# Kernel optimization log

Measured on AMD Instinct MI355X. Metric: run time of the kernel, lower is better.

The kernel has to match this reference:

```python
import jax, jax.numpy as jnp
import numpy as np

BS, SEQ, D, H = 2, 2048, 1024, 16
HD = D // H  # head_dim = 64


def setup_inputs() -> dict:
    key = jax.random.key(0)
    kx, kw = jax.random.split(key)
    x = jax.random.normal(kx, (BS, SEQ, D), dtype=jnp.float32)
    # qkv Linear: weight [3D, D] (xavier_normal), bias zeros
    std = float(np.sqrt(2.0 / (D + 3 * D)))
    W_qkv = jax.random.normal(kw, (3 * D, D), dtype=jnp.float32) * std
    b_qkv = jnp.zeros((3 * D,), dtype=jnp.float32)
    return {"x": x, "W_qkv": W_qkv, "b_qkv": b_qkv}


def reference(x, W_qkv, b_qkv):
    bs, seq_len, embed_dim = x.shape
    # fused QKV projection: [bs, seq, 3D]
    qkv = x @ W_qkv.T + b_qkv
    qkv = qkv.reshape(bs, seq_len, 3, H, HD)
    qkv = jnp.transpose(qkv, (2, 0, 3, 1, 4))  # [3, bs, H, seq, HD]
    Q, K, V = qkv[0], qkv[1], qkv[2]
    # past_kv is None -> total_len == seq_len, past_len == 0
    scores = jnp.einsum("bhqd,bhkd->bhqk", Q, K) / jnp.sqrt(jnp.float32(HD))
    # causal mask: True above diagonal -> -inf
    mask = jnp.triu(jnp.ones((seq_len, seq_len), dtype=bool), k=1)
    scores = jnp.where(mask[None, None, :, :], -jnp.inf, scores)
    probs = jax.nn.softmax(scores, axis=-1)
    # attn_dropout = 0.0 (eval) -> identity
    out = jnp.einsum("bhqk,bhkd->bhqd", probs, V)
    out = jnp.transpose(out, (0, 2, 1, 3)).reshape(bs, seq_len, embed_dim)
    return (out, (K, V))
```

## Files before the change

kernel.cpp:

```cpp
#include <hip/hip_runtime.h>

typedef __bf16 bf16_t;
typedef __bf16 bf16x8 __attribute__((ext_vector_type(8)));
typedef float f32x4 __attribute__((ext_vector_type(4)));

__device__ __forceinline__ bf16_t f2bf(float f) {
  unsigned u = __float_as_uint(f);
  u += 0x7fffu + ((u >> 16) & 1u);
  unsigned short s = (unsigned short)(u >> 16);
  union { unsigned short s; bf16_t b; } cv; cv.s = s; return cv.b;
}

__device__ __forceinline__ void gl16(const void* g, void* l) {
  __builtin_amdgcn_global_load_lds(
      (const __attribute__((address_space(1))) void*)g,
      (__attribute__((address_space(3))) void*)l,
      16, 0, 0);
}

__global__ __launch_bounds__(256) void cvt_kernel(const float* __restrict__ src,
                                                  bf16_t* __restrict__ dst, int n8) {
  int i = blockIdx.x * 256 + threadIdx.x;
  if (i >= n8) return;
  const float4* s = (const float4*)src + (size_t)i * 2;
  float4 a = s[0], b = s[1];
  bf16x8 o;
  o[0] = f2bf(a.x); o[1] = f2bf(a.y); o[2] = f2bf(a.z); o[3] = f2bf(a.w);
  o[4] = f2bf(b.x); o[5] = f2bf(b.y); o[6] = f2bf(b.z); o[7] = f2bf(b.w);
  *((bf16x8*)dst + i) = o;
}

#define GEMM_K 1024
__global__ __launch_bounds__(256) void qkv_gemm(
    const bf16_t* __restrict__ A,
    const bf16_t* __restrict__ B,
    const float* __restrict__ bias,
    float* __restrict__ Ko, float* __restrict__ Vo,
    bf16_t* __restrict__ Qb, bf16_t* __restrict__ Kb,
    bf16_t* __restrict__ Vt)
{
  __shared__ bf16_t lsA[128 * 32];
  __shared__ bf16_t lsB[128 * 32];
  const int tid = threadIdx.x;
  const int lane = tid & 63;
  const int ln = lane & 15, qd = lane >> 4;
  const int wid = tid >> 6;
  const int wm = wid & 1, wn = wid >> 1;
  const int bm = blockIdx.x & 31, bn = blockIdx.x >> 5;
  const int m0 = bm * 128, n0 = bn * 128;

  f32x4 acc[4][4] = {};

  const int c0 = tid, c1 = tid + 256;
  const bf16_t* ga0 = A + (size_t)(m0 + (c0 >> 2)) * GEMM_K + (c0 & 3) * 8;
  const bf16_t* ga1 = A + (size_t)(m0 + (c1 >> 2)) * GEMM_K + (c1 & 3) * 8;
  const bf16_t* gb0 = B + (size_t)(n0 + (c0 >> 2)) * GEMM_K + (c0 & 3) * 8;
  const bf16_t* gb1 = B + (size_t)(n0 + (c1 >> 2)) * GEMM_K + (c1 & 3) * 8;
  bf16_t* la0 = &lsA[c0 * 8];
  bf16_t* la1 = &lsA[c1 * 8];
  bf16_t* lb0 = &lsB[c0 * 8];
  bf16_t* lb1 = &lsB[c1 * 8];

  for (int k0 = 0; k0 < GEMM_K; k0 += 32) {
    __syncthreads();
    gl16(ga0 + k0, la0);
    gl16(ga1 + k0, la1);
    gl16(gb0 + k0, lb0);
    gl16(gb1 + k0, lb1);
    __syncthreads();
    bf16x8 af[4], bf[4];
#pragma unroll
    for (int mi = 0; mi < 4; ++mi)
      af[mi] = *(const bf16x8*)&lsA[(wm * 64 + mi * 16 + ln) * 32 + qd * 8];
#pragma unroll
    for (int ni = 0; ni < 4; ++ni)
      bf[ni] = *(const bf16x8*)&lsB[(wn * 64 + ni * 16 + ln) * 32 + qd * 8];
#pragma unroll
    for (int mi = 0; mi < 4; ++mi)
#pragma unroll
      for (int ni = 0; ni < 4; ++ni)
        acc[mi][ni] = __builtin_amdgcn_mfma_f32_16x16x32_bf16(af[mi], bf[ni], acc[mi][ni], 0, 0, 0);
  }

  const int sec = n0 >> 10;
#pragma unroll
  for (int mi = 0; mi < 4; ++mi) {
#pragma unroll
    for (int ni = 0; ni < 4; ++ni) {
      const int colg = n0 + wn * 64 + ni * 16 + ln;
      const float bv = bias[colg];
      const int cc = colg & 1023, h = cc >> 6, hd = cc & 63;
#pragma unroll
      for (int r = 0; r < 4; ++r) {
        const int mg = m0 + wm * 64 + mi * 16 + qd * 4 + r;
        const int b = mg >> 11, s = mg & 2047;
        const float val = acc[mi][ni][r] + bv;
        const size_t idx = ((size_t)((b * 16 + h) * 2048 + s)) * 64 + hd;
        if (sec == 0) {
          Qb[idx] = f2bf(val);
        } else if (sec == 1) {
          Ko[idx] = val;
          Kb[idx] = f2bf(val);
        } else {
          Vo[idx] = val;
          Vt[((size_t)(b * 16 + h) * 64 + hd) * 2048 + s] = f2bf(val);
        }
      }
    }
  }
}

#define LP_STRIDE 72
__global__ __launch_bounds__(256) void attn_kernel(
    const bf16_t* __restrict__ Qb,
    const bf16_t* __restrict__ Kb,
    const bf16_t* __restrict__ Vt,
    float* __restrict__ Oacc,
    float* __restrict__ lacc)
{
  __shared__ bf16_t lq[128 * 64];
  __shared__ bf16_t lk[64 * 64];
  __shared__ bf16_t lv[64 * 64];
  __shared__ bf16_t lp[128 * LP_STRIDE];
  const int tid = threadIdx.x;
  const int lane = tid & 63, ln = lane & 15, qd = lane >> 4;
  const int w = tid >> 6;

  const int bh = blockIdx.x / 40;
  int c = blockIdx.x % 40;
  int it = 0;
#pragma unroll
  for (int t = 0; t < 16; ++t) {
    int nc = (2 * t + 9) >> 3;
    if (c < nc) { it = t; break; }
    c -= nc;
  }
  const int jt0 = c * 8;
  const int jt1 = min(jt0 + 8, 2 * it + 2);
  const int b = bh >> 4, h = bh & 15;

  const bf16_t* qbase = Qb + (size_t)bh * 2048 * 64 + (size_t)it * 128 * 64;
  const bf16_t* kbase = Kb + (size_t)bh * 2048 * 64;
  const bf16_t* vbase = Vt + (size_t)bh * 64 * 2048;

#pragma unroll
  for (int i = 0; i < 4; ++i) {
    int cc = tid + i * 256;
    gl16(qbase + cc * 8, &lq[cc * 8]);
  }
  __syncthreads();
  bf16x8 afq[2][2];
#pragma unroll
  for (int kk = 0; kk < 2; ++kk)
#pragma unroll
    for (int mi = 0; mi < 2; ++mi)
      afq[kk][mi] = *(const bf16x8*)&lq[(w * 32 + mi * 16 + ln) * 64 + kk * 32 + qd * 8];

  f32x4 oc[2][4] = {};
  float lsum[2][4] = {};
  const float C1 = 0.125f * 1.44269504f;

  for (int jt = jt0; jt < jt1; ++jt) {
    __syncthreads();
    {
      const bf16_t* kt = kbase + (size_t)jt * 64 * 64;
      int cc = tid, c2 = tid + 256;
      gl16(kt + cc * 8, &lk[cc * 8]);
      gl16(kt + c2 * 8, &lk[c2 * 8]);
      gl16(vbase + (size_t)(cc >> 3) * 2048 + jt * 64 + (cc & 7) * 8, &lv[cc * 8]);
      gl16(vbase + (size_t)(c2 >> 3) * 2048 + jt * 64 + (c2 & 7) * 8, &lv[c2 * 8]);
    }
    __syncthreads();

    f32x4 sa[2][4] = {};
#pragma unroll
    for (int kk = 0; kk < 2; ++kk) {
      bf16x8 bfk[4];
#pragma unroll
      for (int ni = 0; ni < 4; ++ni)
        bfk[ni] = *(const bf16x8*)&lk[(ni * 16 + ln) * 64 + kk * 32 + qd * 8];
#pragma unroll
      for (int mi = 0; mi < 2; ++mi)
#pragma unroll
        for (int ni = 0; ni < 4; ++ni)
          sa[mi][ni] = __builtin_amdgcn_mfma_f32_16x16x32_bf16(afq[kk][mi], bfk[ni], sa[mi][ni], 0, 0, 0);
    }

    const bool diag = (jt >= 2 * it);
#pragma unroll
    for (int mi = 0; mi < 2; ++mi) {
#pragma unroll
      for (int r = 0; r < 4; ++r) {
        const int rowg = it * 128 + w * 32 + mi * 16 + qd * 4 + r;
#pragma unroll
        for (int ni = 0; ni < 4; ++ni) {
          float sv = sa[mi][ni][r] * C1;
          if (diag) {
            int colg = jt * 64 + ni * 16 + ln;
            if (colg > rowg) sv = -10000.f;
          }
          float p = __builtin_amdgcn_exp2f(sv);
          sa[mi][ni][r] = p;
          lsum[mi][r] += p;
        }
      }
    }

#pragma unroll
    for (int mi = 0; mi < 2; ++mi)
#pragma unroll
      for (int ni = 0; ni < 4; ++ni)
#pragma unroll
        for (int r = 0; r < 4; ++r)
          lp[(w * 32 + mi * 16 + qd * 4 + r) * LP_STRIDE + ni * 16 + ln] = f2bf(sa[mi][ni][r]);

#pragma unroll
    for (int kk = 0; kk < 2; ++kk) {
      bf16x8 afp[2], bfv[4];
#pragma unroll
      for (int mi = 0; mi < 2; ++mi)
        afp[mi] = *(const bf16x8*)&lp[(w * 32 + mi * 16 + ln) * LP_STRIDE + kk * 32 + qd * 8];
#pragma unroll
      for (int ni = 0; ni < 4; ++ni)
        bfv[ni] = *(const bf16x8*)&lv[(ni * 16 + ln) * 64 + kk * 32 + qd * 8];
#pragma unroll
      for (int mi = 0; mi < 2; ++mi)
#pragma unroll
        for (int ni = 0; ni < 4; ++ni)
          oc[mi][ni] = __builtin_amdgcn_mfma_f32_16x16x32_bf16(afp[mi], bfv[ni], oc[mi][ni], 0, 0, 0);
    }
  }

#pragma unroll
  for (int mi = 0; mi < 2; ++mi) {
#pragma unroll
    for (int r = 0; r < 4; ++r) {
      float ls = lsum[mi][r];
      ls += __shfl_xor(ls, 1);
      ls += __shfl_xor(ls, 2);
      ls += __shfl_xor(ls, 4);
      ls += __shfl_xor(ls, 8);
      const int rowg = it * 128 + w * 32 + mi * 16 + qd * 4 + r;
      if (ln == 0) atomicAdd(lacc + bh * 2048 + rowg, ls);
#pragma unroll
      for (int ni = 0; ni < 4; ++ni) {
        const int colh = ni * 16 + ln;
        atomicAdd(Oacc + (size_t)(b * 2048 + rowg) * 1024 + h * 64 + colh, oc[mi][ni][r]);
      }
    }
  }
}

__global__ __launch_bounds__(256) void norm_kernel(float* __restrict__ Oacc,
                                                   const float* __restrict__ lacc) {
  const size_t f = ((size_t)blockIdx.x * 256 + threadIdx.x) * 4;
  const int d = (int)(f & 1023);
  const int s = (int)((f >> 10) & 2047);
  const int b = (int)(f >> 21);
  const int h = d >> 6;
  const float l = lacc[(((size_t)b * 16 + h) << 11) | s];
  const float inv = 1.0f / l;
  float4* p = (float4*)(Oacc + f);
  float4 v = *p;
  v.x *= inv; v.y *= inv; v.z *= inv; v.w *= inv;
  *p = v;
}

extern "C" void kernel_launch(void* const* d_in, const int* in_sizes, int n_in,
                              void* d_out, int out_size, void* d_ws, size_t ws_size,
                              hipStream_t stream) {
  const float* x = (const float*)d_in[0];
  const float* W = (const float*)d_in[1];
  const float* bq = (const float*)d_in[2];
  float* out = (float*)d_out;
  float* Ko = out + 4194304;
  float* Vo = out + 8388608;
  char* ws = (char*)d_ws;
  bf16_t* xb = (bf16_t*)ws;
  bf16_t* wb = (bf16_t*)(ws + 8388608);
  bf16_t* Qb = (bf16_t*)(ws + 14680064);
  bf16_t* Kb = (bf16_t*)(ws + 23068672);
  bf16_t* Vt = (bf16_t*)(ws + 31457280);
  float*  lacc = (float*)(ws + 39845888);

  hipMemsetAsync(out, 0, 4194304 * sizeof(float), stream);
  hipMemsetAsync(lacc, 0, 65536 * sizeof(float), stream);
  hipLaunchKernelGGL(cvt_kernel, dim3(2048), dim3(256), 0, stream, x, xb, 524288);
  hipLaunchKernelGGL(cvt_kernel, dim3(1536), dim3(256), 0, stream, W, wb, 393216);
  hipLaunchKernelGGL(qkv_gemm, dim3(768), dim3(256), 0, stream, xb, wb, bq, Ko, Vo, Qb, Kb, Vt);
  hipLaunchKernelGGL(attn_kernel, dim3(1280), dim3(256), 0, stream, Qb, Kb, Vt, out, lacc);
  hipLaunchKernelGGL(norm_kernel, dim3(4096), dim3(256), 0, stream, out, lacc);
}
```

Baseline: 195.0 us.

## Swizzle LDS layouts, tile K/V contiguously, drop split-K attention atomics and norm pass

Converted inputs and the GEMM's Q/K/V outputs are written in XOR-swizzled, 64-row tiled layouts, so LDS fragment reads avoid bank conflicts and K/V tiles load as contiguous chunks. The attention kernel no longer splits the key range across blocks. Each of the 512 blocks handles one full query tile in longest-first order and writes normalized output directly. This removes the memsets, the atomicAdd reductions and the separate norm kernel. The cost is fewer blocks with unbalanced per-block work, which may lower parallelism on the tail.

```diff
diff --git a/kernel.cpp b/kernel.cpp
--- a/kernel.cpp
+++ b/kernel.cpp
@@ -27,7 +27,10 @@
   bf16x8 o;
   o[0] = f2bf(a.x); o[1] = f2bf(a.y); o[2] = f2bf(a.z); o[3] = f2bf(a.w);
   o[4] = f2bf(b.x); o[5] = f2bf(b.y); o[6] = f2bf(b.z); o[7] = f2bf(b.w);
-  *((bf16x8*)dst + i) = o;
+  const int row = i >> 7, jr = i & 127;
+  const int g = jr >> 2, jj = jr & 3;
+  const int dstc = (row << 7) + (g << 2) + (jj ^ ((row >> 1) & 3));
+  *((bf16x8*)dst + dstc) = o;
 }
 
 #define GEMM_K 1024
@@ -48,6 +51,7 @@
   const int wm = wid & 1, wn = wid >> 1;
   const int bm = blockIdx.x & 31, bn = blockIdx.x >> 5;
   const int m0 = bm * 128, n0 = bn * 128;
+  const int qs = qd ^ ((ln >> 1) & 3);
 
   f32x4 acc[4][4] = {};
 
@@ -71,10 +75,10 @@
     bf16x8 af[4], bf[4];
 #pragma unroll
     for (int mi = 0; mi < 4; ++mi)
-      af[mi] = *(const bf16x8*)&lsA[(wm * 64 + mi * 16 + ln) * 32 + qd * 8];
+      af[mi] = *(const bf16x8*)&lsA[(wm * 64 + mi * 16 + ln) * 32 + qs * 8];
 #pragma unroll
     for (int ni = 0; ni < 4; ++ni)
-      bf[ni] = *(const bf16x8*)&lsB[(wn * 64 + ni * 16 + ln) * 32 + qd * 8];
+      bf[ni] = *(const bf16x8*)&lsB[(wn * 64 + ni * 16 + ln) * 32 + qs * 8];
 #pragma unroll
     for (int mi = 0; mi < 4; ++mi)
 #pragma unroll
@@ -95,15 +99,20 @@
         const int mg = m0 + wm * 64 + mi * 16 + qd * 4 + r;
         const int b = mg >> 11, s = mg & 2047;
         const float val = acc[mi][ni][r] + bv;
-        const size_t idx = ((size_t)((b * 16 + h) * 2048 + s)) * 64 + hd;
+        const int bhi = b * 16 + h;
+        const size_t pidx = ((size_t)(bhi * 2048 + s)) * 64 + hd;
+        const size_t sidx = (size_t)bhi * 131072 + (size_t)(s >> 6) * 4096 +
+                            (size_t)(s & 63) * 64 + (((hd >> 3) ^ (s & 7)) << 3) + (hd & 7);
         if (sec == 0) {
-          Qb[idx] = f2bf(val);
+          Qb[sidx] = f2bf(val);
         } else if (sec == 1) {
-          Ko[idx] = val;
-          Kb[idx] = f2bf(val);
+          Ko[pidx] = val;
+          Kb[sidx] = f2bf(val);
         } else {
-          Vo[idx] = val;
-          Vt[((size_t)(b * 16 + h) * 64 + hd) * 2048 + s] = f2bf(val);
+          Vo[pidx] = val;
+          const size_t vidx = (size_t)bhi * 131072 + (size_t)(s >> 6) * 4096 +
+                              (size_t)hd * 64 + ((((s >> 3) & 7) ^ (hd & 7)) << 3) + (s & 7);
+          Vt[vidx] = f2bf(val);
         }
       }
     }
@@ -115,8 +124,7 @@
     const bf16_t* __restrict__ Qb,
     const bf16_t* __restrict__ Kb,
     const bf16_t* __restrict__ Vt,
-    float* __restrict__ Oacc,
-    float* __restrict__ lacc)
+    float* __restrict__ Out)
 {
   __shared__ bf16_t lq[128 * 64];
   __shared__ bf16_t lk[64 * 64];
@@ -126,22 +134,15 @@
   const int lane = tid & 63, ln = lane & 15, qd = lane >> 4;
   const int w = tid >> 6;
 
-  const int bh = blockIdx.x / 40;
-  int c = blockIdx.x % 40;
-  int it = 0;
-#pragma unroll
-  for (int t = 0; t < 16; ++t) {
-    int nc = (2 * t + 9) >> 3;
-    if (c < nc) { it = t; break; }
-    c -= nc;
-  }
-  const int jt0 = c * 8;
-  const int jt1 = min(jt0 + 8, 2 * it + 2);
+  const int bidx = blockIdx.x;
+  const int bh = bidx & 31;
+  const int x = bidx >> 5;
+  const int it = (bidx < 256) ? (15 - x) : (x - 8);
   const int b = bh >> 4, h = bh & 15;
 
-  const bf16_t* qbase = Qb + (size_t)bh * 2048 * 64 + (size_t)it * 128 * 64;
-  const bf16_t* kbase = Kb + (size_t)bh * 2048 * 64;
-  const bf16_t* vbase = Vt + (size_t)bh * 64 * 2048;
+  const bf16_t* qbase = Qb + (size_t)bh * 131072 + (size_t)it * 8192;
+  const bf16_t* kbase = Kb + (size_t)bh * 131072;
+  const bf16_t* vbase = Vt + (size_t)bh * 131072;
 
 #pragma unroll
   for (int i = 0; i < 4; ++i) {
@@ -153,22 +154,27 @@
 #pragma unroll
   for (int kk = 0; kk < 2; ++kk)
 #pragma unroll
-    for (int mi = 0; mi < 2; ++mi)
-      afq[kk][mi] = *(const bf16x8*)&lq[(w * 32 + mi * 16 + ln) * 64 + kk * 32 + qd * 8];
+    for (int mi = 0; mi < 2; ++mi) {
+      const int row = w * 32 + mi * 16 + ln;
+      afq[kk][mi] = *(const bf16x8*)&lq[(row >> 6) * 4096 + (row & 63) * 64 +
+                                        (((kk * 4 + qd) ^ (ln & 7)) << 3)];
+    }
 
   f32x4 oc[2][4] = {};
   float lsum[2][4] = {};
   const float C1 = 0.125f * 1.44269504f;
 
-  for (int jt = jt0; jt < jt1; ++jt) {
+  const int jt1 = 2 * it + 2;
+  for (int jt = 0; jt < jt1; ++jt) {
     __syncthreads();
     {
-      const bf16_t* kt = kbase + (size_t)jt * 64 * 64;
+      const bf16_t* kt = kbase + (size_t)jt * 4096;
+      const bf16_t* vt = vbase + (size_t)jt * 4096;
       int cc = tid, c2 = tid + 256;
       gl16(kt + cc * 8, &lk[cc * 8]);
       gl16(kt + c2 * 8, &lk[c2 * 8]);
-      gl16(vbase + (size_t)(cc >> 3) * 2048 + jt * 64 + (cc & 7) * 8, &lv[cc * 8]);
-      gl16(vbase + (size_t)(c2 >> 3) * 2048 + jt * 64 + (c2 & 7) * 8, &lv[c2 * 8]);
+      gl16(vt + cc * 8, &lv[cc * 8]);
+      gl16(vt + c2 * 8, &lv[c2 * 8]);
     }
     __syncthreads();
 
@@ -178,7 +184,7 @@
       bf16x8 bfk[4];
 #pragma unroll
       for (int ni = 0; ni < 4; ++ni)
-        bfk[ni] = *(const bf16x8*)&lk[(ni * 16 + ln) * 64 + kk * 32 + qd * 8];
+        bfk[ni] = *(const bf16x8*)&lk[(ni * 16 + ln) * 64 + (((kk * 4 + qd) ^ (ln & 7)) << 3)];
 #pragma unroll
       for (int mi = 0; mi < 2; ++mi)
 #pragma unroll
@@ -222,7 +228,7 @@
         afp[mi] = *(const bf16x8*)&lp[(w * 32 + mi * 16 + ln) * LP_STRIDE + kk * 32 + qd * 8];
 #pragma unroll
       for (int ni = 0; ni < 4; ++ni)
-        bfv[ni] = *(const bf16x8*)&lv[(ni * 16 + ln) * 64 + kk * 32 + qd * 8];
+        bfv[ni] = *(const bf16x8*)&lv[(ni * 16 + ln) * 64 + (((kk * 4 + qd) ^ (ln & 7)) << 3)];
 #pragma unroll
       for (int mi = 0; mi < 2; ++mi)
 #pragma unroll
@@ -240,30 +246,15 @@
       ls += __shfl_xor(ls, 2);
       ls += __shfl_xor(ls, 4);
       ls += __shfl_xor(ls, 8);
-      const int rowg = it * 128 + w * 32 + mi * 16 + qd * 4 + r;
-      if (ln == 0) atomicAdd(lacc + bh * 2048 + rowg, ls);
+      const float inv = 1.0f / ls;
+      const int rowq = it * 128 + w * 32 + mi * 16 + qd * 4 + r;
 #pragma unroll
       for (int ni = 0; ni < 4; ++ni) {
         const int colh = ni * 16 + ln;
-        atomicAdd(Oacc + (size_t)(b * 2048 + rowg) * 1024 + h * 64 + colh, oc[mi][ni][r]);
+        Out[(size_t)(b * 2048 + rowq) * 1024 + h * 64 + colh] = oc[mi][ni][r] * inv;
       }
     }
   }
-}
-
-__global__ __launch_bounds__(256) void norm_kernel(float* __restrict__ Oacc,
-                                                   const float* __restrict__ lacc) {
-  const size_t f = ((size_t)blockIdx.x * 256 + threadIdx.x) * 4;
-  const int d = (int)(f & 1023);
-  const int s = (int)((f >> 10) & 2047);
-  const int b = (int)(f >> 21);
-  const int h = d >> 6;
-  const float l = lacc[(((size_t)b * 16 + h) << 11) | s];
-  const float inv = 1.0f / l;
-  float4* p = (float4*)(Oacc + f);
-  float4 v = *p;
-  v.x *= inv; v.y *= inv; v.z *= inv; v.w *= inv;
-  *p = v;
 }
 
 extern "C" void kernel_launch(void* const* d_in, const int* in_sizes, int n_in,
@@ -281,13 +272,9 @@
   bf16_t* Qb = (bf16_t*)(ws + 14680064);
   bf16_t* Kb = (bf16_t*)(ws + 23068672);
   bf16_t* Vt = (bf16_t*)(ws + 31457280);
-  float*  lacc = (float*)(ws + 39845888);
-
-  hipMemsetAsync(out, 0, 4194304 * sizeof(float), stream);
-  hipMemsetAsync(lacc, 0, 65536 * sizeof(float), stream);
+
   hipLaunchKernelGGL(cvt_kernel, dim3(2048), dim3(256), 0, stream, x, xb, 524288);
   hipLaunchKernelGGL(cvt_kernel, dim3(1536), dim3(256), 0, stream, W, wb, 393216);
   hipLaunchKernelGGL(qkv_gemm, dim3(768), dim3(256), 0, stream, xb, wb, bq, Ko, Vo, Qb, Kb, Vt);
-  hipLaunchKernelGGL(attn_kernel, dim3(1280), dim3(256), 0, stream, Qb, Kb, Vt, out, lacc);
-  hipLaunchKernelGGL(norm_kernel, dim3(4096), dim3(256), 0, stream, out, lacc);
-}
+  hipLaunchKernelGGL(attn_kernel, dim3(512), dim3(256), 0, stream, Qb, Kb, Vt, out);
+}
```

Result: no change. 191.6 us (-1.7%).
